# Optimization experiments

Measured on AMD Instinct MI355X. Metric: run time of the kernel, lower is better.

The kernel has to match this reference:

```python
import jax, jax.numpy as jnp
import numpy as np

B, S, E = 8, 2048, 768
U = 1024          # cfc_units (total NCP units; motor neurons = first E)
BB = 512          # CfC backbone width
H_MLP = 4 * E

def _lecun_tanh(x):
    return 1.7159 * jnp.tanh(0.666 * x)

def _layernorm(x, g, b, eps=1e-5):
    mu = jnp.mean(x, axis=-1, keepdims=True)
    var = jnp.var(x, axis=-1, keepdims=True)
    return (x - mu) * jax.lax.rsqrt(var + eps) * g + b


def setup_inputs() -> dict:
    key = jax.random.key(0)
    ks = jax.random.split(key, 16)
    sc = 0.02
    d = {}
    d["x"] = jax.random.normal(ks[0], (B, S, E), dtype=jnp.float32)
    d["hx"] = jnp.zeros((B, U), dtype=jnp.float32)
    # ln_1 / ln_2
    d["ln1_g"] = jnp.ones((E,), jnp.float32); d["ln1_b"] = jnp.zeros((E,), jnp.float32)
    d["ln2_g"] = jnp.ones((E,), jnp.float32); d["ln2_b"] = jnp.zeros((E,), jnp.float32)
    # CfC cell (default mode): backbone over concat([input, h]) then ff1/ff2/time_a/time_b heads
    d["W_bb"] = sc * jax.random.normal(ks[1], (E + U, BB), jnp.float32)
    d["b_bb"] = jnp.zeros((BB,), jnp.float32)
    d["W_ff1"] = sc * jax.random.normal(ks[2], (BB, U), jnp.float32)
    d["b_ff1"] = jnp.zeros((U,), jnp.float32)
    d["W_ff2"] = sc * jax.random.normal(ks[3], (BB, U), jnp.float32)
    d["b_ff2"] = jnp.zeros((U,), jnp.float32)
    d["W_ta"] = sc * jax.random.normal(ks[4], (BB, U), jnp.float32)
    d["b_ta"] = jnp.zeros((U,), jnp.float32)
    d["W_tb"] = sc * jax.random.normal(ks[5], (BB, U), jnp.float32)
    d["b_tb"] = jnp.zeros((U,), jnp.float32)
    # LIF gate params (per n_embd unit)
    d["lif_thr"] = jnp.full((E,), 0.01, jnp.float32)
    d["lif_leak"] = jnp.full((E,), 2.0, jnp.float32)
    d["lif_steep"] = jnp.full((E,), 2.0, jnp.float32)
    # MLP
    d["W1"] = sc * jax.random.normal(ks[6], (E, H_MLP), jnp.float32)
    d["b1"] = jnp.zeros((H_MLP,), jnp.float32)
    d["W2"] = sc * jax.random.normal(ks[7], (H_MLP, E), jnp.float32)
    d["b2"] = jnp.zeros((E,), jnp.float32)
    return d


def _cfc_scan(normed, hx, W_bb, b_bb, W_ff1, b_ff1, W_ff2, b_ff2, W_ta, b_ta, W_tb, b_tb):
    # normed: [B, S, E]; hx: [B, U]. Closed-form continuous-time cell, ts=1.
    xs = jnp.swapaxes(normed, 0, 1)  # [S, B, E]

    def step(h, x_t):
        cat = jnp.concatenate([x_t, h], axis=-1)           # [B, E+U]
        bb = _lecun_tanh(cat @ W_bb + b_bb)                # [B, BB]
        ff1 = _lecun_tanh(bb @ W_ff1 + b_ff1)              # [B, U]
        ff2 = _lecun_tanh(bb @ W_ff2 + b_ff2)
        t_interp = jax.nn.sigmoid((bb @ W_ta + b_ta) + (bb @ W_tb + b_tb))
        h_new = ff1 * (1.0 - t_interp) + t_interp * ff2    # [B, U]
        return h_new, h_new[:, :E]                         # motor neurons -> output

    new_hx, ys = jax.lax.scan(step, hx, xs)
    return jnp.swapaxes(ys, 0, 1), new_hx                  # [B, S, E], [B, U]


def _lif_gate(x, thr, leak, steep):
    threshold = jnp.abs(thr) * 0.1
    leak_s = jax.nn.sigmoid(leak)
    steepness = jax.nn.softplus(steep)
    potential = jnp.abs(x)
    fire = jax.nn.sigmoid(steepness * (potential - threshold))
    gate = fire + leak_s * (1.0 - fire)
    return x * gate


def reference(x, hx, ln1_g, ln1_b, ln2_g, ln2_b,
              W_bb, b_bb, W_ff1, b_ff1, W_ff2, b_ff2, W_ta, b_ta, W_tb, b_tb,
              lif_thr, lif_leak, lif_steep, W1, b1, W2, b2):
    normed = _layernorm(x, ln1_g, ln1_b)
    cfc_out, new_hx = _cfc_scan(normed, hx, W_bb, b_bb, W_ff1, b_ff1,
                                W_ff2, b_ff2, W_ta, b_ta, W_tb, b_tb)
    cfc_out = _lif_gate(cfc_out, lif_thr, lif_leak, lif_steep)
    x = x + cfc_out  # dropout = identity in eval
    h2 = _layernorm(x, ln2_g, ln2_b)
    mlp = jax.nn.gelu(h2 @ W1 + b1, approximate=False) @ W2 + b2
    x = x + mlp
    return x, new_hx
```

## Files before the change

kernel.cpp:

```cpp
#include <hip/hip_runtime.h>
#include <math.h>

#define NB 8
#define NS 2048
#define NE 768
#define NU 1024
#define NBB 512
#define NH 3072
#define NBS (NB*NS)

typedef float f32x4v __attribute__((ext_vector_type(4)));
typedef __bf16 bf16x8v __attribute__((ext_vector_type(8)));
typedef unsigned short u16x8v __attribute__((ext_vector_type(8)));
typedef unsigned short u16x4v __attribute__((ext_vector_type(4)));

__device__ __forceinline__ unsigned short f2bf(float f) {
  unsigned int u = __builtin_bit_cast(unsigned int, f);
  u = (u + 0x7fffu + ((u >> 16) & 1u)) >> 16;
  return (unsigned short)u;
}
__device__ __forceinline__ float bf2f(unsigned short h) {
  unsigned int u = ((unsigned int)h) << 16;
  return __builtin_bit_cast(float, u);
}

__device__ __forceinline__ float ald(const float* p) {
  return __hip_atomic_load((const float*)p, __ATOMIC_RELAXED, __HIP_MEMORY_SCOPE_AGENT);
}
__device__ __forceinline__ void ast(float* p, float v) {
  __hip_atomic_store(p, v, __ATOMIC_RELAXED, __HIP_MEMORY_SCOPE_AGENT);
}
__device__ __forceinline__ unsigned aldu(const unsigned* p) {
  return __hip_atomic_load(p, __ATOMIC_RELAXED, __HIP_MEMORY_SCOPE_AGENT);
}
__device__ __forceinline__ void astu(unsigned* p, unsigned v) {
  __hip_atomic_store(p, v, __ATOMIC_RELAXED, __HIP_MEMORY_SCOPE_AGENT);
}
__device__ __forceinline__ float4 ald4(const float* p) {
  float4 v;
  asm volatile("global_load_dwordx4 %0, %1, off sc0 sc1"
               : "=v"(v) : "v"(p) : "memory");
  return v;
}
__device__ __forceinline__ void wait_vmcnt0() {
  asm volatile("s_waitcnt vmcnt(0)" ::: "memory");
  __builtin_amdgcn_sched_barrier(0);
}

__global__ __launch_bounds__(256) void tr_f32(const float* __restrict__ in,
                                              float* __restrict__ out, int R, int C) {
  __shared__ float tile[32][33];
  int c0 = blockIdx.x * 32, r0 = blockIdx.y * 32;
  int tx = threadIdx.x, ty = threadIdx.y;
  #pragma unroll
  for (int i = 0; i < 32; i += 8)
    tile[ty + i][tx] = in[(long)(r0 + ty + i) * C + c0 + tx];
  __syncthreads();
  #pragma unroll
  for (int i = 0; i < 32; i += 8)
    out[(long)(c0 + ty + i) * R + r0 + tx] = tile[tx][ty + i];
}

__global__ __launch_bounds__(256) void tr_f32_bf16(const float* __restrict__ in,
                                                   unsigned short* __restrict__ out, int R, int C) {
  __shared__ float tile[32][33];
  int c0 = blockIdx.x * 32, r0 = blockIdx.y * 32;
  int tx = threadIdx.x, ty = threadIdx.y;
  #pragma unroll
  for (int i = 0; i < 32; i += 8)
    tile[ty + i][tx] = in[(long)(r0 + ty + i) * C + c0 + tx];
  __syncthreads();
  #pragma unroll
  for (int i = 0; i < 32; i += 8)
    out[(long)(c0 + ty + i) * R + r0 + tx] = f2bf(tile[tx][ty + i]);
}

__global__ __launch_bounds__(256) void tr_f32_bf16split(const float* __restrict__ in,
    unsigned short* __restrict__ oh, unsigned short* __restrict__ ol, int R, int C) {
  __shared__ float tile[32][33];
  int c0 = blockIdx.x * 32, r0 = blockIdx.y * 32;
  int tx = threadIdx.x, ty = threadIdx.y;
  #pragma unroll
  for (int i = 0; i < 32; i += 8)
    tile[ty + i][tx] = in[(long)(r0 + ty + i) * C + c0 + tx];
  __syncthreads();
  #pragma unroll
  for (int i = 0; i < 32; i += 8) {
    float v = tile[tx][ty + i];
    unsigned short h = f2bf(v);
    long idx = (long)(c0 + ty + i) * R + r0 + tx;
    oh[idx] = h;
    ol[idx] = f2bf(v - bf2f(h));
  }
}

__global__ __launch_bounds__(256) void ln_kernel(const float* __restrict__ in,
    const float* __restrict__ gw, const float* __restrict__ bw,
    unsigned short* __restrict__ outh, unsigned short* __restrict__ outl) {
  int lane = threadIdx.x & 63;
  long row = (long)blockIdx.x * 4 + (threadIdx.x >> 6);
  const float4* rp = (const float4*)(in + row * NE);
  float4 v[3];
  float s = 0.f, sq = 0.f;
  #pragma unroll
  for (int j = 0; j < 3; ++j) {
    v[j] = rp[lane + j * 64];
    s += v[j].x + v[j].y + v[j].z + v[j].w;
    sq += v[j].x*v[j].x + v[j].y*v[j].y + v[j].z*v[j].z + v[j].w*v[j].w;
  }
  #pragma unroll
  for (int m = 1; m < 64; m <<= 1) { s += __shfl_xor(s, m); sq += __shfl_xor(sq, m); }
  float mu = s * (1.f / NE);
  float rs = rsqrtf(sq * (1.f / NE) - mu * mu + 1e-5f);
  #pragma unroll
  for (int j = 0; j < 3; ++j) {
    int c4 = lane + j * 64;
    float4 g4 = ((const float4*)gw)[c4];
    float4 b4 = ((const float4*)bw)[c4];
    float f0 = (v[j].x - mu) * rs * g4.x + b4.x;
    float f1 = (v[j].y - mu) * rs * g4.y + b4.y;
    float f2 = (v[j].z - mu) * rs * g4.z + b4.z;
    float f3 = (v[j].w - mu) * rs * g4.w + b4.w;
    u16x4v oh, ol;
    oh[0] = f2bf(f0); ol[0] = f2bf(f0 - bf2f(oh[0]));
    oh[1] = f2bf(f1); ol[1] = f2bf(f1 - bf2f(oh[1]));
    oh[2] = f2bf(f2); ol[2] = f2bf(f2 - bf2f(oh[2]));
    oh[3] = f2bf(f3); ol[3] = f2bf(f3 - bf2f(oh[3]));
    *(u16x4v*)(outh + row * NE + (long)c4 * 4) = oh;
    *(u16x4v*)(outl + row * NE + (long)c4 * 4) = ol;
  }
}

template<int EPI>
__global__ __launch_bounds__(256) void gemm_bf16(
    const unsigned short* __restrict__ A, const unsigned short* __restrict__ Bt,
    const float* __restrict__ bias, const float* res,
    float* Cf, unsigned short* Cb, int M, int N, int K)
{
  __shared__ unsigned short lA[128][72];
  __shared__ unsigned short lB[128][72];
  int tid = threadIdx.x;
  int lane = tid & 63, wave = tid >> 6;
  int wr = wave >> 1, wc = wave & 1;
  int r15 = lane & 15, hi = lane >> 4;
  int ntn = N >> 7;
  long m0 = (long)(blockIdx.x / ntn) << 7;
  long n0 = (long)(blockIdx.x % ntn) << 7;
  f32x4v acc[4][4];
  #pragma unroll
  for (int m = 0; m < 4; ++m)
    #pragma unroll
    for (int n = 0; n < 4; ++n) acc[m][n] = (f32x4v){0.f, 0.f, 0.f, 0.f};

  for (int kt = 0; kt < K; kt += 64) {
    u16x8v ra[4], rb[4];
    #pragma unroll
    for (int i = 0; i < 4; ++i) {
      int c = tid + (i << 8);
      int rw = c >> 3, ko = (c & 7) << 3;
      ra[i] = *(const u16x8v*)(A + (m0 + rw) * K + kt + ko);
      rb[i] = *(const u16x8v*)(Bt + (n0 + rw) * K + kt + ko);
    }
    __syncthreads();
    #pragma unroll
    for (int i = 0; i < 4; ++i) {
      int c = tid + (i << 8);
      int rw = c >> 3, ko = (c & 7) << 3;
      *(u16x8v*)(&lA[rw][ko]) = ra[i];
      *(u16x8v*)(&lB[rw][ko]) = rb[i];
    }
    __syncthreads();
    #pragma unroll
    for (int ks = 0; ks < 64; ks += 32) {
      bf16x8v af[4], bfr[4];
      #pragma unroll
      for (int m = 0; m < 4; ++m)
        af[m] = *(const bf16x8v*)(&lA[wr * 64 + m * 16 + r15][ks + hi * 8]);
      #pragma unroll
      for (int n = 0; n < 4; ++n)
        bfr[n] = *(const bf16x8v*)(&lB[wc * 64 + n * 16 + r15][ks + hi * 8]);
      #pragma unroll
      for (int m = 0; m < 4; ++m)
        #pragma unroll
        for (int n = 0; n < 4; ++n)
          acc[m][n] = __builtin_amdgcn_mfma_f32_16x16x32_bf16(af[m], bfr[n], acc[m][n], 0, 0, 0);
    }
  }
  #pragma unroll
  for (int m = 0; m < 4; ++m) {
    long rbase = m0 + wr * 64 + m * 16 + hi * 4;
    #pragma unroll
    for (int n = 0; n < 4; ++n) {
      long cg = n0 + wc * 64 + n * 16 + r15;
      float bs = (EPI == 3) ? 0.f : bias[cg];
      #pragma unroll
      for (int e = 0; e < 4; ++e) {
        long row = rbase + e;
        float vv = acc[m][n][e] + bs;
        if (EPI == 0) {
          Cf[row * N + cg] = vv;
        } else if (EPI == 1) {
          float gl = 0.5f * vv * (1.f + erff(vv * 0.70710678118f));
          Cb[row * N + cg] = f2bf(gl);
        } else if (EPI == 2) {
          Cf[row * N + cg] = vv + res[row * N + cg];
        } else {
          Cf[row * N + cg] += vv;
        }
      }
    }
  }
}

__global__ __launch_bounds__(512) void scan_kernel(
    const float* __restrict__ pre, const float* __restrict__ WhhT,
    const float* __restrict__ WhT,
    const float* __restrict__ bf1, const float* __restrict__ bf2,
    const float* __restrict__ bta, const float* __restrict__ btb,
    const float* __restrict__ hx,
    float* hbuf, float* bbf, float* __restrict__ cfc,
    unsigned* doneV, unsigned* doneJ)
{
  __shared__ float lsd[NB * NU];
  __shared__ float lpre[4096];
  __shared__ float lpart[8][4][2][8];
  int tid = threadIdx.x;
  int lane = tid & 63, wave = tid >> 6;
  int bx = blockIdx.x;
  const float4* ls4 = (const float4*)lsd;
  float4* ls4w = (float4*)lsd;

  if (bx < 64) {
    int jb = bx;
    int j1 = (jb << 3) + wave;
    const float4* W14 = (const float4*)(WhhT + (long)j1 * NU);
    float4 wreg[4];
    #pragma unroll
    for (int c = 0; c < 4; ++c) wreg[c] = W14[(c << 6) + lane];
    const unsigned* mycell = doneV + ((jb << 10) + (lane << 4));

    for (int t = 0; t < NS; ++t) {
      if ((t & 63) == 0) {
        int b = tid >> 6, tq = tid & 63;
        const float* src = pre + ((long)b * NS + t + tq) * NBB + (jb << 3);
        float4 p0 = *(const float4*)src;
        float4 p1 = *(const float4*)(src + 4);
        *(float4*)(&lpre[tid * 8])     = p0;
        *(float4*)(&lpre[tid * 8 + 4]) = p1;
      }
      if (wave == 0) {
        while (aldu(mycell) < (unsigned)(t + 1)) {}
      }
      __syncthreads();
      {
        float4 rv[4];
        #pragma unroll
        for (int i = 0; i < 4; ++i) rv[i] = ald4(&hbuf[(((i << 9) + tid) << 2)]);
        wait_vmcnt0();
        #pragma unroll
        for (int i = 0; i < 4; ++i) ls4w[(i << 9) + tid] = rv[i];
      }
      __syncthreads();
      float a1[8];
      #pragma unroll
      for (int b = 0; b < 8; ++b) a1[b] = 0.f;
      #pragma unroll
      for (int c = 0; c < 4; ++c) {
        int idx = (c << 6) + lane;
        float4 w = wreg[c];
        #pragma unroll
        for (int b = 0; b < 8; ++b) {
          float4 hv = ls4[(b << 8) + idx];
          a1[b] += w.x * hv.x + w.y * hv.y + w.z * hv.z + w.w * hv.w;
        }
      }
      #pragma unroll
      for (int m = 1; m < 64; m <<= 1)
        #pragma unroll
        for (int b = 0; b < 8; ++b) a1[b] += __shfl_xor(a1[b], m);
      if (lane < 8) {
        int tq = t & 63;
        float s = a1[lane] + lpre[((lane << 6) + tq) * 8 + wave];
        ast(&bbf[lane * NBB + j1], 1.7159f * tanhf(0.666f * s));
      }
      __syncthreads();
      if (wave == 0)
        astu(doneJ + ((lane << 10) + (jb << 4)), (unsigned)(t + 1));
    }
  } else {
    int vb = bx - 64;
    int head = lane >> 4, v2 = (lane >> 3) & 1, jsub = lane & 7;
    int vg = (vb << 4) + (wave << 1) + v2;
    const float4* W24 = (const float4*)(WhT + ((long)head * NU + vg) * NBB);
    float4 w2reg[16];
    #pragma unroll
    for (int c = 0; c < 16; ++c) w2reg[c] = W24[(c << 3) + jsub];
    int vl = tid >> 3, bq = tid & 7;
    int wv = vl >> 1, qq = vl & 1;
    int vo = (vb << 4) + vl;
    float cb1 = 0.f, cb2 = 0.f, cbt = 0.f;
    if (tid < 128) { cb1 = bf1[vo]; cb2 = bf2[vo]; cbt = bta[vo] + btb[vo]; }
    const unsigned* mycell = doneJ + ((vb << 10) + (lane << 4));

    if (tid < 128) ast(&hbuf[bq * NU + vo], hx[bq * NU + vo]);
    __syncthreads();
    if (wave == 0)
      astu(doneV + ((lane << 10) + (vb << 4)), 1u);

    for (int t = 0; t < NS; ++t) {
      if (wave == 0) {
        while (aldu(mycell) < (unsigned)(t + 1)) {}
      }
      __syncthreads();
      {
        float4 rv[2];
        #pragma unroll
        for (int i = 0; i < 2; ++i) rv[i] = ald4(&bbf[(((i << 9) + tid) << 2)]);
        wait_vmcnt0();
        #pragma unroll
        for (int i = 0; i < 2; ++i) ls4w[(i << 9) + tid] = rv[i];
      }
      __syncthreads();
      float a2[8];
      #pragma unroll
      for (int b = 0; b < 8; ++b) a2[b] = 0.f;
      #pragma unroll
      for (int c = 0; c < 16; ++c) {
        int idx = (c << 3) + jsub;
        float4 w = w2reg[c];
        #pragma unroll
        for (int b = 0; b < 8; ++b) {
          float4 bv = ls4[(b << 7) + idx];
          a2[b] += w.x * bv.x + w.y * bv.y + w.z * bv.z + w.w * bv.w;
        }
      }
      #pragma unroll
      for (int m = 1; m < 8; m <<= 1)
        #pragma unroll
        for (int b = 0; b < 8; ++b) a2[b] += __shfl_xor(a2[b], m);
      if (jsub == 0) {
        #pragma unroll
        for (int b = 0; b < 8; ++b) lpart[wave][head][v2][b] = a2[b];
      }
      __syncthreads();
      float hn = 0.f;
      if (tid < 128) {
        float d1 = lpart[wv][0][qq][bq] + cb1;
        float d2 = lpart[wv][1][qq][bq] + cb2;
        float dt = lpart[wv][2][qq][bq] + lpart[wv][3][qq][bq] + cbt;
        float f1 = 1.7159f * tanhf(0.666f * d1);
        float f2 = 1.7159f * tanhf(0.666f * d2);
        float ti = 1.f / (1.f + expf(-dt));
        hn = f1 * (1.f - ti) + ti * f2;
        ast(&hbuf[bq * NU + vo], hn);
      }
      __syncthreads();
      if (wave == 0)
        astu(doneV + ((lane << 10) + (vb << 4)), (unsigned)(t + 2));
      if (tid < 128 && vo < NE) cfc[((long)bq * NS + t) * NE + vo] = hn;
    }
  }
}

__global__ __launch_bounds__(256) void lif_kernel(
    const float* __restrict__ x, const float* __restrict__ cfc,
    const float* __restrict__ thr, const float* __restrict__ leak,
    const float* __restrict__ steep, const float* __restrict__ hbuf,
    float* __restrict__ x1, float* __restrict__ outTail)
{
  long i4 = (long)blockIdx.x * blockDim.x + threadIdx.x;
  float4 xv = ((const float4*)x)[i4];
  float4 cv = ((const float4*)cfc)[i4];
  int col = (int)((i4 << 2) % NE);
  float4 tv = *(const float4*)(thr + col);
  float4 lv = *(const float4*)(leak + col);
  float4 sv = *(const float4*)(steep + col);
  float4 r;
#define LIF1(comp) { \
    float th = fabsf(tv.comp) * 0.1f; \
    float ls = 1.f / (1.f + expf(-lv.comp)); \
    float sp = (sv.comp > 20.f) ? sv.comp : log1pf(expf(sv.comp)); \
    float fire = 1.f / (1.f + expf(-sp * (fabsf(cv.comp) - th))); \
    float gate = fire + ls * (1.f - fire); \
    r.comp = xv.comp + cv.comp * gate; }
  LIF1(x) LIF1(y) LIF1(z) LIF1(w)
#undef LIF1
  ((float4*)x1)[i4] = r;
  if (i4 < (NB * NU / 4)) {
    const float* hp = hbuf + (i4 << 2);
    float4 hv; hv.x = ald(hp); hv.y = ald(hp + 1); hv.z = ald(hp + 2); hv.w = ald(hp + 3);
    ((float4*)outTail)[i4] = hv;
  }
}

extern "C" void kernel_launch(void* const* d_in, const int* in_sizes, int n_in,
                              void* d_out, int out_size, void* d_ws, size_t ws_size,
                              hipStream_t stream) {
  (void)in_sizes; (void)n_in; (void)out_size; (void)ws_size;
  const float* x     = (const float*)d_in[0];
  const float* hx    = (const float*)d_in[1];
  const float* ln1g  = (const float*)d_in[2];
  const float* ln1b  = (const float*)d_in[3];
  const float* ln2g  = (const float*)d_in[4];
  const float* ln2b  = (const float*)d_in[5];
  const float* Wbb   = (const float*)d_in[6];
  const float* bbb   = (const float*)d_in[7];
  const float* Wff1  = (const float*)d_in[8];
  const float* bff1  = (const float*)d_in[9];
  const float* Wff2  = (const float*)d_in[10];
  const float* bff2  = (const float*)d_in[11];
  const float* Wta   = (const float*)d_in[12];
  const float* btaP  = (const float*)d_in[13];
  const float* Wtb   = (const float*)d_in[14];
  const float* btbP  = (const float*)d_in[15];
  const float* lthr  = (const float*)d_in[16];
  const float* lleak = (const float*)d_in[17];
  const float* lstp  = (const float*)d_in[18];
  const float* W1    = (const float*)d_in[19];
  const float* b1    = (const float*)d_in[20];
  const float* W2    = (const float*)d_in[21];
  const float* b2    = (const float*)d_in[22];

  char* base = (char*)d_ws;
  unsigned short* normedH = (unsigned short*)base;
  float* pre   = (float*)(base + 25165824);
  float* cfc   = (float*)(base + 58720256);
  unsigned short* gelu = (unsigned short*)base;
  unsigned short* normedL = (unsigned short*)(base + 109051904);
  unsigned short* h2      = (unsigned short*)(base + 109051904);
  unsigned* doneV = (unsigned*)(base + 125829120);
  unsigned* doneJ = (unsigned*)(base + 126091264);
  unsigned short* wtbbH = (unsigned short*)(base + 134217728);
  float* whhT  = (float*)(base + 135004160);
  float* whT   = (float*)(base + 137101312);
  unsigned short* w1t = (unsigned short*)(base + 145489920);
  unsigned short* w2t = (unsigned short*)(base + 150208512);
  float* hbuf  = (float*)(base + 154927104);
  float* bbf   = (float*)(base + 154959872);
  unsigned short* wtbbL = (unsigned short*)(base + 154980352);
  float* xout  = (float*)d_out;
  float* outTail = xout + (size_t)NBS * NE;
  unsigned short* lnlo_dummy = (unsigned short*)base;

  dim3 b328(32, 8);
  tr_f32_bf16split<<<dim3(512/32, 768/32), b328, 0, stream>>>(Wbb, wtbbH, wtbbL, 768, 512);
  tr_f32<<<dim3(512/32, 1024/32), b328, 0, stream>>>(Wbb + 768*512, whhT, 1024, 512);
  tr_f32<<<dim3(1024/32, 512/32), b328, 0, stream>>>(Wff1, whT + 0*(size_t)NU*NBB, 512, 1024);
  tr_f32<<<dim3(1024/32, 512/32), b328, 0, stream>>>(Wff2, whT + 1*(size_t)NU*NBB, 512, 1024);
  tr_f32<<<dim3(1024/32, 512/32), b328, 0, stream>>>(Wta,  whT + 2*(size_t)NU*NBB, 512, 1024);
  tr_f32<<<dim3(1024/32, 512/32), b328, 0, stream>>>(Wtb,  whT + 3*(size_t)NU*NBB, 512, 1024);
  tr_f32_bf16<<<dim3(3072/32, 768/32), b328, 0, stream>>>(W1, w1t, 768, 3072);
  tr_f32_bf16<<<dim3(768/32, 3072/32), b328, 0, stream>>>(W2, w2t, 3072, 768);

  ln_kernel<<<NBS/4, 256, 0, stream>>>(x, ln1g, ln1b, normedH, normedL);
  gemm_bf16<0><<<(NBS/128)*(NBB/128), 256, 0, stream>>>(normedH, wtbbH, bbb, nullptr,
                                                        pre, nullptr, NBS, NBB, NE);
  gemm_bf16<3><<<(NBS/128)*(NBB/128), 256, 0, stream>>>(normedH, wtbbL, bbb, nullptr,
                                                        pre, nullptr, NBS, NBB, NE);
  gemm_bf16<3><<<(NBS/128)*(NBB/128), 256, 0, stream>>>(normedL, wtbbH, bbb, nullptr,
                                                        pre, nullptr, NBS, NBB, NE);

  hipMemsetAsync(doneV, 0, 524288, stream);

  scan_kernel<<<128, 512, 0, stream>>>(pre, whhT, whT, bff1, bff2, btaP, btbP, hx,
                                       hbuf, bbf, cfc, doneV, doneJ);

  lif_kernel<<<(NBS*NE/4)/256, 256, 0, stream>>>(x, cfc, lthr, lleak, lstp, hbuf, xout, outTail);
  ln_kernel<<<NBS/4, 256, 0, stream>>>(xout, ln2g, ln2b, h2, lnlo_dummy);
  gemm_bf16<1><<<(NBS/128)*(NH/128), 256, 0, stream>>>(h2, w1t, b1, nullptr,
                                                       nullptr, gelu, NBS, NH, NE);
  gemm_bf16<2><<<(NBS/128)*(NE/128), 256, 0, stream>>>(gelu, w2t, b2, xout,
                                                       xout, nullptr, NBS, NE, NH);
}
```

Before: 17.28 ms.

## Replace scan flag counters with tagged data words for inter-block handoff

The persistent scan kernel drops its separate done-counter arrays. The step index is instead embedded in the low 8 mantissa bits of each exchanged float, so consumers poll the data itself with sc0/sc1 vector loads and retry until the tags match. This removes one flag write, the extra barriers and a dependent load round trip per timestep between the two block groups, and it pads the shared-memory layouts. The cost is truncating 8 mantissa bits of the hidden-state and backbone values (precision loss), plus spin-polling of data lines.

```diff
diff --git a/kernel.cpp b/kernel.cpp
--- a/kernel.cpp
+++ b/kernel.cpp
@@ -10,6 +10,7 @@
 #define NBS (NB*NS)
 
 typedef float f32x4v __attribute__((ext_vector_type(4)));
+typedef unsigned u32x4v __attribute__((ext_vector_type(4)));
 typedef __bf16 bf16x8v __attribute__((ext_vector_type(8)));
 typedef unsigned short u16x8v __attribute__((ext_vector_type(8)));
 typedef unsigned short u16x4v __attribute__((ext_vector_type(4)));
@@ -30,14 +31,8 @@
 __device__ __forceinline__ void ast(float* p, float v) {
   __hip_atomic_store(p, v, __ATOMIC_RELAXED, __HIP_MEMORY_SCOPE_AGENT);
 }
-__device__ __forceinline__ unsigned aldu(const unsigned* p) {
-  return __hip_atomic_load(p, __ATOMIC_RELAXED, __HIP_MEMORY_SCOPE_AGENT);
-}
-__device__ __forceinline__ void astu(unsigned* p, unsigned v) {
-  __hip_atomic_store(p, v, __ATOMIC_RELAXED, __HIP_MEMORY_SCOPE_AGENT);
-}
-__device__ __forceinline__ float4 ald4(const float* p) {
-  float4 v;
+__device__ __forceinline__ f32x4v ald4(const float* p) {
+  f32x4v v;
   asm volatile("global_load_dwordx4 %0, %1, off sc0 sc1"
                : "=v"(v) : "v"(p) : "memory");
   return v;
@@ -45,6 +40,20 @@
 __device__ __forceinline__ void wait_vmcnt0() {
   asm volatile("s_waitcnt vmcnt(0)" ::: "memory");
   __builtin_amdgcn_sched_barrier(0);
+}
+__device__ __forceinline__ void ast4_tag(float* p, float a, float b,
+                                         float c, float d, unsigned tag) {
+  u32x4v u;
+  u.x = (__builtin_bit_cast(unsigned, a) & 0xFFFFFF00u) | tag;
+  u.y = (__builtin_bit_cast(unsigned, b) & 0xFFFFFF00u) | tag;
+  u.z = (__builtin_bit_cast(unsigned, c) & 0xFFFFFF00u) | tag;
+  u.w = (__builtin_bit_cast(unsigned, d) & 0xFFFFFF00u) | tag;
+  asm volatile("global_store_dwordx4 %0, %1, off sc0 sc1"
+               :: "v"(p), "v"(u) : "memory");
+}
+__device__ __forceinline__ unsigned tagbad(f32x4v v, unsigned tag) {
+  u32x4v u = __builtin_bit_cast(u32x4v, v);
+  return ((u.x ^ tag) | (u.y ^ tag) | (u.z ^ tag) | (u.w ^ tag)) & 0xFFu;
 }
 
 __global__ __launch_bounds__(256) void tr_f32(const float* __restrict__ in,
@@ -218,17 +227,16 @@
     const float* __restrict__ bf1, const float* __restrict__ bf2,
     const float* __restrict__ bta, const float* __restrict__ btb,
     const float* __restrict__ hx,
-    float* hbuf, float* bbf, float* __restrict__ cfc,
-    unsigned* doneV, unsigned* doneJ)
+    float* hbuf2, float* bb2, float* __restrict__ cfc, float* hfin)
 {
-  __shared__ float lsd[NB * NU];
+  __shared__ float lsd[8 * 1032];
   __shared__ float lpre[4096];
   __shared__ float lpart[8][4][2][8];
+  __shared__ float hstage[128];
   int tid = threadIdx.x;
   int lane = tid & 63, wave = tid >> 6;
   int bx = blockIdx.x;
   const float4* ls4 = (const float4*)lsd;
-  float4* ls4w = (float4*)lsd;
 
   if (bx < 64) {
     int jb = bx;
@@ -237,9 +245,9 @@
     float4 wreg[4];
     #pragma unroll
     for (int c = 0; c < 4; ++c) wreg[c] = W14[(c << 6) + lane];
-    const unsigned* mycell = doneV + ((jb << 10) + (lane << 4));
 
     for (int t = 0; t < NS; ++t) {
+      unsigned tagc = (unsigned)(t & 255);
       if ((t & 63) == 0) {
         int b = tid >> 6, tq = tid & 63;
         const float* src = pre + ((long)b * NS + t + tq) * NBB + (jb << 3);
@@ -248,17 +256,36 @@
         *(float4*)(&lpre[tid * 8])     = p0;
         *(float4*)(&lpre[tid * 8 + 4]) = p1;
       }
-      if (wave == 0) {
-        while (aldu(mycell) < (unsigned)(t + 1)) {}
+      f32x4v rv0, rv1, rv2, rv3;
+      {
+        unsigned need = 0xFu;
+        do {
+          if (need & 1u) rv0 = ald4(hbuf2 + tid * 16);
+          if (need & 2u) rv1 = ald4(hbuf2 + tid * 16 + 4);
+          if (need & 4u) rv2 = ald4(hbuf2 + tid * 16 + 8);
+          if (need & 8u) rv3 = ald4(hbuf2 + tid * 16 + 12);
+          wait_vmcnt0();
+          unsigned nn = 0;
+          if ((need & 1u) && tagbad(rv0, tagc)) nn |= 1u;
+          if ((need & 2u) && tagbad(rv1, tagc)) nn |= 2u;
+          if ((need & 4u) && tagbad(rv2, tagc)) nn |= 4u;
+          if ((need & 8u) && tagbad(rv3, tagc)) nn |= 8u;
+          need = nn;
+          if (need) __builtin_amdgcn_s_sleep(1);
+        } while (need);
       }
       __syncthreads();
       {
-        float4 rv[4];
-        #pragma unroll
-        for (int i = 0; i < 4; ++i) rv[i] = ald4(&hbuf[(((i << 9) + tid) << 2)]);
-        wait_vmcnt0();
-        #pragma unroll
-        for (int i = 0; i < 4; ++i) ls4w[(i << 9) + tid] = rv[i];
+        int v0 = tid * 2;
+        lsd[0*1032 + v0] = rv0.x; lsd[1*1032 + v0] = rv0.y;
+        lsd[2*1032 + v0] = rv0.z; lsd[3*1032 + v0] = rv0.w;
+        lsd[4*1032 + v0] = rv1.x; lsd[5*1032 + v0] = rv1.y;
+        lsd[6*1032 + v0] = rv1.z; lsd[7*1032 + v0] = rv1.w;
+        int v1 = v0 + 1;
+        lsd[0*1032 + v1] = rv2.x; lsd[1*1032 + v1] = rv2.y;
+        lsd[2*1032 + v1] = rv2.z; lsd[3*1032 + v1] = rv2.w;
+        lsd[4*1032 + v1] = rv3.x; lsd[5*1032 + v1] = rv3.y;
+        lsd[6*1032 + v1] = rv3.z; lsd[7*1032 + v1] = rv3.w;
       }
       __syncthreads();
       float a1[8];
@@ -270,7 +297,7 @@
         float4 w = wreg[c];
         #pragma unroll
         for (int b = 0; b < 8; ++b) {
-          float4 hv = ls4[(b << 8) + idx];
+          float4 hv = ls4[b * 258 + idx];
           a1[b] += w.x * hv.x + w.y * hv.y + w.z * hv.z + w.w * hv.w;
         }
       }
@@ -278,14 +305,17 @@
       for (int m = 1; m < 64; m <<= 1)
         #pragma unroll
         for (int b = 0; b < 8; ++b) a1[b] += __shfl_xor(a1[b], m);
-      if (lane < 8) {
-        int tq = t & 63;
-        float s = a1[lane] + lpre[((lane << 6) + tq) * 8 + wave];
-        ast(&bbf[lane * NBB + j1], 1.7159f * tanhf(0.666f * s));
-      }
-      __syncthreads();
-      if (wave == 0)
-        astu(doneJ + ((lane << 10) + (jb << 4)), (unsigned)(t + 1));
+      {
+        int bsel = lane & 7, tq = t & 63;
+        float s = a1[bsel] + lpre[((bsel << 6) + tq) * 8 + wave];
+        float tb_ = 1.7159f * tanhf(0.666f * s);
+        float g0 = __shfl(tb_, 0), g1 = __shfl(tb_, 1);
+        float g2 = __shfl(tb_, 2), g3 = __shfl(tb_, 3);
+        float g4 = __shfl(tb_, 4), g5 = __shfl(tb_, 5);
+        float g6 = __shfl(tb_, 6), g7 = __shfl(tb_, 7);
+        if (lane == 0) ast4_tag(bb2 + j1 * 8,     g0, g1, g2, g3, tagc);
+        if (lane == 1) ast4_tag(bb2 + j1 * 8 + 4, g4, g5, g6, g7, tagc);
+      }
     }
   } else {
     int vb = bx - 64;
@@ -300,25 +330,38 @@
     int vo = (vb << 4) + vl;
     float cb1 = 0.f, cb2 = 0.f, cbt = 0.f;
     if (tid < 128) { cb1 = bf1[vo]; cb2 = bf2[vo]; cbt = bta[vo] + btb[vo]; }
-    const unsigned* mycell = doneJ + ((vb << 10) + (lane << 4));
-
-    if (tid < 128) ast(&hbuf[bq * NU + vo], hx[bq * NU + vo]);
+
+    if (tid < 128) hstage[vl * 8 + bq] = hx[bq * NU + vo];
     __syncthreads();
-    if (wave == 0)
-      astu(doneV + ((lane << 10) + (vb << 4)), 1u);
+    if (tid < 32) {
+      int vloc = tid >> 1, hf = tid & 1;
+      const float* s = &hstage[vloc * 8 + hf * 4];
+      ast4_tag(hbuf2 + ((vb << 4) + vloc) * 8 + hf * 4,
+               s[0], s[1], s[2], s[3], 0u);
+    }
 
     for (int t = 0; t < NS; ++t) {
-      if (wave == 0) {
-        while (aldu(mycell) < (unsigned)(t + 1)) {}
+      unsigned tagc = (unsigned)(t & 255);
+      f32x4v rv0, rv1;
+      {
+        unsigned need = 3u;
+        do {
+          if (need & 1u) rv0 = ald4(bb2 + tid * 8);
+          if (need & 2u) rv1 = ald4(bb2 + tid * 8 + 4);
+          wait_vmcnt0();
+          unsigned nn = 0;
+          if ((need & 1u) && tagbad(rv0, tagc)) nn |= 1u;
+          if ((need & 2u) && tagbad(rv1, tagc)) nn |= 2u;
+          need = nn;
+          if (need) __builtin_amdgcn_s_sleep(1);
+        } while (need);
       }
       __syncthreads();
       {
-        float4 rv[2];
-        #pragma unroll
-        for (int i = 0; i < 2; ++i) rv[i] = ald4(&bbf[(((i << 9) + tid) << 2)]);
-        wait_vmcnt0();
-        #pragma unroll
-        for (int i = 0; i < 2; ++i) ls4w[(i << 9) + tid] = rv[i];
+        lsd[0*520 + tid] = rv0.x; lsd[1*520 + tid] = rv0.y;
+        lsd[2*520 + tid] = rv0.z; lsd[3*520 + tid] = rv0.w;
+        lsd[4*520 + tid] = rv1.x; lsd[5*520 + tid] = rv1.y;
+        lsd[6*520 + tid] = rv1.z; lsd[7*520 + tid] = rv1.w;
       }
       __syncthreads();
       float a2[8];
@@ -330,7 +373,7 @@
         float4 w = w2reg[c];
         #pragma unroll
         for (int b = 0; b < 8; ++b) {
-          float4 bv = ls4[(b << 7) + idx];
+          float4 bv = ls4[b * 130 + idx];
           a2[b] += w.x * bv.x + w.y * bv.y + w.z * bv.z + w.w * bv.w;
         }
       }
@@ -352,11 +395,19 @@
         float f2 = 1.7159f * tanhf(0.666f * d2);
         float ti = 1.f / (1.f + expf(-dt));
         hn = f1 * (1.f - ti) + ti * f2;
-        ast(&hbuf[bq * NU + vo], hn);
+        hstage[vl * 8 + bq] = hn;
       }
       __syncthreads();
-      if (wave == 0)
-        astu(doneV + ((lane << 10) + (vb << 4)), (unsigned)(t + 2));
+      if (t + 1 < NS) {
+        if (tid < 32) {
+          int vloc = tid >> 1, hf = tid & 1;
+          const float* s = &hstage[vloc * 8 + hf * 4];
+          ast4_tag(hbuf2 + ((vb << 4) + vloc) * 8 + hf * 4,
+                   s[0], s[1], s[2], s[3], (unsigned)((t + 1) & 255));
+        }
+      } else {
+        if (tid < 128) ast(&hfin[bq * NU + vo], hn);
+      }
       if (tid < 128 && vo < NE) cfc[((long)bq * NS + t) * NE + vo] = hn;
     }
   }
@@ -365,7 +416,7 @@
 __global__ __launch_bounds__(256) void lif_kernel(
     const float* __restrict__ x, const float* __restrict__ cfc,
     const float* __restrict__ thr, const float* __restrict__ leak,
-    const float* __restrict__ steep, const float* __restrict__ hbuf,
+    const float* __restrict__ steep, const float* __restrict__ hfin,
     float* __restrict__ x1, float* __restrict__ outTail)
 {
   long i4 = (long)blockIdx.x * blockDim.x + threadIdx.x;
@@ -387,7 +438,7 @@
 #undef LIF1
   ((float4*)x1)[i4] = r;
   if (i4 < (NB * NU / 4)) {
-    const float* hp = hbuf + (i4 << 2);
+    const float* hp = hfin + (i4 << 2);
     float4 hv; hv.x = ald(hp); hv.y = ald(hp + 1); hv.z = ald(hp + 2); hv.w = ald(hp + 3);
     ((float4*)outTail)[i4] = hv;
   }
@@ -428,15 +479,14 @@
   unsigned short* gelu = (unsigned short*)base;
   unsigned short* normedL = (unsigned short*)(base + 109051904);
   unsigned short* h2      = (unsigned short*)(base + 109051904);
-  unsigned* doneV = (unsigned*)(base + 125829120);
-  unsigned* doneJ = (unsigned*)(base + 126091264);
+  float* hfin = (float*)(base + 125829120);
   unsigned short* wtbbH = (unsigned short*)(base + 134217728);
   float* whhT  = (float*)(base + 135004160);
   float* whT   = (float*)(base + 137101312);
   unsigned short* w1t = (unsigned short*)(base + 145489920);
   unsigned short* w2t = (unsigned short*)(base + 150208512);
-  float* hbuf  = (float*)(base + 154927104);
-  float* bbf   = (float*)(base + 154959872);
+  float* hbuf2 = (float*)(base + 154927104);
+  float* bb2   = (float*)(base + 154959872);
   unsigned short* wtbbL = (unsigned short*)(base + 154980352);
   float* xout  = (float*)d_out;
   float* outTail = xout + (size_t)NBS * NE;
@@ -460,12 +510,12 @@
   gemm_bf16<3><<<(NBS/128)*(NBB/128), 256, 0, stream>>>(normedL, wtbbH, bbb, nullptr,
                                                         pre, nullptr, NBS, NBB, NE);
 
-  hipMemsetAsync(doneV, 0, 524288, stream);
+  (void)hipMemsetAsync(hbuf2, 0xAA, 49152, stream);
 
   scan_kernel<<<128, 512, 0, stream>>>(pre, whhT, whT, bff1, bff2, btaP, btbP, hx,
-                                       hbuf, bbf, cfc, doneV, doneJ);
-
-  lif_kernel<<<(NBS*NE/4)/256, 256, 0, stream>>>(x, cfc, lthr, lleak, lstp, hbuf, xout, outTail);
+                                       hbuf2, bb2, cfc, hfin);
+
+  lif_kernel<<<(NBS*NE/4)/256, 256, 0, stream>>>(x, cfc, lthr, lleak, lstp, hfin, xout, outTail);
   ln_kernel<<<NBS/4, 256, 0, stream>>>(xout, ln2g, ln2b, h2, lnlo_dummy);
   gemm_bf16<1><<<(NBS/128)*(NH/128), 256, 0, stream>>>(h2, w1t, b1, nullptr,
                                                        nullptr, gelu, NBS, NH, NE);
```

Result: slower. 24.76 ms (+43.3%).

## Signal per-wave completion flags in scan to drop a block barrier

Applied to the files above, without the earlier changes.

In the backbone blocks of the persistent scan kernel, each wave now waits for its own stores and writes its own completion flag, which replaces the trailing block-wide barrier and the single flag per block. Consumer blocks poll eight per-wave flags per lane, reduce them with a wave-wide min, and sleep briefly between polls. The flag array is enlarged to match, and the periodic pre-activation prefetch now runs after the wait instead of before it. The goal is to shorten the critical path of each sequential timestep, at the cost of more flag traffic and heavier polling per step.

```diff
diff --git a/kernel.cpp b/kernel.cpp
--- a/kernel.cpp
+++ b/kernel.cpp
@@ -36,8 +36,8 @@
 __device__ __forceinline__ void astu(unsigned* p, unsigned v) {
   __hip_atomic_store(p, v, __ATOMIC_RELAXED, __HIP_MEMORY_SCOPE_AGENT);
 }
-__device__ __forceinline__ float4 ald4(const float* p) {
-  float4 v;
+__device__ __forceinline__ f32x4v ald4(const float* p) {
+  f32x4v v;
   asm volatile("global_load_dwordx4 %0, %1, off sc0 sc1"
                : "=v"(v) : "v"(p) : "memory");
   return v;
@@ -240,25 +240,26 @@
     const unsigned* mycell = doneV + ((jb << 10) + (lane << 4));
 
     for (int t = 0; t < NS; ++t) {
+      if (wave == 0) {
+        while (aldu(mycell) < (unsigned)(t + 1)) {}
+      }
+      __syncthreads();
       if ((t & 63) == 0) {
         int b = tid >> 6, tq = tid & 63;
         const float* src = pre + ((long)b * NS + t + tq) * NBB + (jb << 3);
-        float4 p0 = *(const float4*)src;
+        float4 p0 = *(const float4*)(src);
         float4 p1 = *(const float4*)(src + 4);
         *(float4*)(&lpre[tid * 8])     = p0;
         *(float4*)(&lpre[tid * 8 + 4]) = p1;
       }
-      if (wave == 0) {
-        while (aldu(mycell) < (unsigned)(t + 1)) {}
-      }
-      __syncthreads();
       {
-        float4 rv[4];
+        f32x4v rv[4];
         #pragma unroll
         for (int i = 0; i < 4; ++i) rv[i] = ald4(&hbuf[(((i << 9) + tid) << 2)]);
         wait_vmcnt0();
         #pragma unroll
-        for (int i = 0; i < 4; ++i) ls4w[(i << 9) + tid] = rv[i];
+        for (int i = 0; i < 4; ++i)
+          ls4w[(i << 9) + tid] = (float4){rv[i].x, rv[i].y, rv[i].z, rv[i].w};
       }
       __syncthreads();
       float a1[8];
@@ -283,9 +284,8 @@
         float s = a1[lane] + lpre[((lane << 6) + tq) * 8 + wave];
         ast(&bbf[lane * NBB + j1], 1.7159f * tanhf(0.666f * s));
       }
-      __syncthreads();
-      if (wave == 0)
-        astu(doneJ + ((lane << 10) + (jb << 4)), (unsigned)(t + 1));
+      wait_vmcnt0();
+      astu(doneJ + ((lane << 13) + (((jb << 3) + wave) << 4)), (unsigned)(t + 1));
     }
   } else {
     int vb = bx - 64;
@@ -300,7 +300,6 @@
     int vo = (vb << 4) + vl;
     float cb1 = 0.f, cb2 = 0.f, cbt = 0.f;
     if (tid < 128) { cb1 = bf1[vo]; cb2 = bf2[vo]; cbt = bta[vo] + btb[vo]; }
-    const unsigned* mycell = doneJ + ((vb << 10) + (lane << 4));
 
     if (tid < 128) ast(&hbuf[bq * NU + vo], hx[bq * NU + vo]);
     __syncthreads();
@@ -309,16 +308,35 @@
 
     for (int t = 0; t < NS; ++t) {
       if (wave == 0) {
-        while (aldu(mycell) < (unsigned)(t + 1)) {}
+        const unsigned* pb = doneJ + ((vb << 13) + (lane << 7));
+        unsigned tgt = (unsigned)(t + 1);
+        unsigned m;
+        do {
+          unsigned c0 = aldu(pb),       c1 = aldu(pb + 16);
+          unsigned c2 = aldu(pb + 32),  c3 = aldu(pb + 48);
+          unsigned c4 = aldu(pb + 64),  c5 = aldu(pb + 80);
+          unsigned c6 = aldu(pb + 96),  c7 = aldu(pb + 112);
+          unsigned a = c0 < c1 ? c0 : c1, b2 = c2 < c3 ? c2 : c3;
+          unsigned c = c4 < c5 ? c4 : c5, d = c6 < c7 ? c6 : c7;
+          m = a < b2 ? a : b2; unsigned n = c < d ? c : d;
+          m = m < n ? m : n;
+          #pragma unroll
+          for (int s = 1; s < 64; s <<= 1) {
+            unsigned o = __shfl_xor(m, s);
+            m = m < o ? m : o;
+          }
+          if (m < tgt) __builtin_amdgcn_s_sleep(1);
+        } while (m < tgt);
       }
       __syncthreads();
       {
-        float4 rv[2];
+        f32x4v rv[2];
         #pragma unroll
         for (int i = 0; i < 2; ++i) rv[i] = ald4(&bbf[(((i << 9) + tid) << 2)]);
         wait_vmcnt0();
         #pragma unroll
-        for (int i = 0; i < 2; ++i) ls4w[(i << 9) + tid] = rv[i];
+        for (int i = 0; i < 2; ++i)
+          ls4w[(i << 9) + tid] = (float4){rv[i].x, rv[i].y, rv[i].z, rv[i].w};
       }
       __syncthreads();
       float a2[8];
@@ -460,7 +478,7 @@
   gemm_bf16<3><<<(NBS/128)*(NBB/128), 256, 0, stream>>>(normedL, wtbbH, bbb, nullptr,
                                                         pre, nullptr, NBS, NBB, NE);
 
-  hipMemsetAsync(doneV, 0, 524288, stream);
+  (void)hipMemsetAsync(doneV, 0, 262144 + 2097152, stream);
 
   scan_kernel<<<128, 512, 0, stream>>>(pre, whhT, whT, bff1, bff2, btaP, btbP, hx,
                                        hbuf, bbf, cfc, doneV, doneJ);
```

Result: slower. 22.38 ms (+29.5%).
